# Kernel optimization log

Hardware: AMD Instinct MI355X
Metric: run time of the kernel (lower is better)

The kernel has to match this reference:

```python
import jax, jax.numpy as jnp
import numpy as np

B = 1024
N_SPEC = 2048
R1 = 20000
R2 = 40000


def setup_inputs() -> dict:
    key = jax.random.key(0)
    k1, k2, k3, k4, k5, k6, k7 = jax.random.split(key, 7)
    return {
        "y_in": jax.random.uniform(k1, (B, N_SPEC), dtype=jnp.float32),
        "rates_1st": jax.random.uniform(k2, (B, R1), dtype=jnp.float32),
        "rates_2nd": jax.random.uniform(k3, (B, R2), dtype=jnp.float32),
        "inds_1r": jax.random.randint(k4, (R1,), 0, N_SPEC, dtype=jnp.int32),
        "inds_1p": jax.random.randint(k5, (R1,), 0, N_SPEC, dtype=jnp.int32),
        "inds_2r": jax.random.randint(k6, (R2, 2), 0, N_SPEC, dtype=jnp.int32),
        "inds_2p": jax.random.randint(k7, (R2,), 0, N_SPEC, dtype=jnp.int32),
    }


def reference(y_in, rates_1st, rates_2nd, inds_1r, inds_1p, inds_2r, inds_2p):
    # First-order reactions: gather reactant abundance, scale by rate,
    # scatter-add into product species.  y_in: [B, S]
    term_1 = y_in[:, inds_1r] * rates_1st                      # [B, R1]
    # Second-order reactions: product of the two reactant abundances.
    term_2 = y_in[:, inds_2r[:, 0]] * y_in[:, inds_2r[:, 1]] * rates_2nd  # [B, R2]
    y_out = jnp.zeros_like(y_in)
    y_out = y_out.at[:, inds_1p].add(term_1)
    y_out = y_out.at[:, inds_2p].add(term_2)
    return y_out
```

## Files before the change

### kernel.cpp

```cpp
#include <hip/hip_runtime.h>


#define NSPEC 2048
#define BDIM  1024
#define R1    20000
#define R2    40000
#define CH    10000
#define NCH1  2
#define NCH2  4
#define NCH   (NCH1 + NCH2)
#define RTOT  (R1 + R2)

#define WS_CNT  0
#define WS_PTR  49152
#define WS_E1   98432
#define WS_E2   178560

__global__ __launch_bounds__(256) void k_zero(uint* cnt) {
    int i = blockIdx.x * 256 + threadIdx.x;
    if (i < NCH * NSPEC) cnt[i] = 0u;
}

__global__ __launch_bounds__(256) void k_hist(const int* __restrict__ inds_1p,
                                              const int* __restrict__ inds_2p,
                                              uint* __restrict__ cnt) {
    int j = blockIdx.x * 256 + threadIdx.x;
    if (j >= RTOT) return;
    if (j < R1) {
        int c = j / CH;
        atomicAdd(&cnt[c * NSPEC + inds_1p[j]], 1u);
    } else {
        int j2 = j - R1;
        int c = NCH1 + j2 / CH;
        atomicAdd(&cnt[c * NSPEC + inds_2p[j2]], 1u);
    }
}

__global__ __launch_bounds__(256) void k_scan(uint* __restrict__ cnt,
                                              uint* __restrict__ ptr) {
    __shared__ uint part[256];
    const int c   = blockIdx.x;
    const int tid = threadIdx.x;
    uint v[8];
    uint tsum = 0;
    #pragma unroll
    for (int k = 0; k < 8; ++k) { v[k] = cnt[c * NSPEC + tid * 8 + k]; tsum += v[k]; }
    part[tid] = tsum;
    __syncthreads();
    for (int off = 1; off < 256; off <<= 1) {
        uint x = (tid >= off) ? part[tid - off] : 0u;
        __syncthreads();
        part[tid] += x;
        __syncthreads();
    }
    uint run = part[tid] - tsum;
    #pragma unroll
    for (int k = 0; k < 8; ++k) {
        ptr[c * (NSPEC + 1) + tid * 8 + k] = run;
        cnt[c * NSPEC + tid * 8 + k]       = run;
        run += v[k];
    }
    if (tid == 255) ptr[c * (NSPEC + 1) + NSPEC] = run;
}

__global__ __launch_bounds__(256) void k_fill(const int* __restrict__ inds_1r,
                                              const int* __restrict__ inds_1p,
                                              const int* __restrict__ inds_2r,
                                              const int* __restrict__ inds_2p,
                                              uint*  __restrict__ cur,
                                              uint*  __restrict__ e1,
                                              uint2* __restrict__ e2) {
    int j = blockIdx.x * 256 + threadIdx.x;
    if (j >= RTOT) return;
    if (j < R1) {
        int c = j / CH;
        int s = inds_1p[j];
        uint pos = atomicAdd(&cur[c * NSPEC + s], 1u);
        uint jl  = (uint)(j - c * CH);
        e1[c * CH + pos] = (uint)inds_1r[j] | (jl << 16);
    } else {
        int j2 = j - R1;
        int c  = j2 / CH;
        int s  = inds_2p[j2];
        uint pos = atomicAdd(&cur[(NCH1 + c) * NSPEC + s], 1u);
        uint jl  = (uint)(j2 - c * CH);
        uint r0  = (uint)inds_2r[2 * j2];
        uint r1_ = (uint)inds_2r[2 * j2 + 1];
        e2[c * CH + pos] = make_uint2(r0 | (r1_ << 16), jl);
    }
}

#define MBLOCK 512
#define SPT    (NSPEC / MBLOCK)

__global__ __launch_bounds__(MBLOCK) void k_main(
    const float* __restrict__ y_in,
    const float* __restrict__ rates_1st,
    const float* __restrict__ rates_2nd,
    const uint*  __restrict__ ptr,
    const uint*  __restrict__ e1,
    const uint2* __restrict__ e2,
    float*       __restrict__ y_out)
{
    __shared__ float ys[NSPEC];
    __shared__ float rl[CH];

    const int b   = blockIdx.x;
    const int tid = threadIdx.x;

    {
        const float4* yrow = reinterpret_cast<const float4*>(y_in + (size_t)b * NSPEC);
        reinterpret_cast<float4*>(ys)[tid] = yrow[tid];
    }

    float acc[SPT];
    #pragma unroll
    for (int k = 0; k < SPT; ++k) acc[k] = 0.f;

    for (int c = 0; c < NCH; ++c) {
        const float* src = (c < NCH1)
            ? rates_1st + (size_t)b * R1 + c * CH
            : rates_2nd + (size_t)b * R2 + (c - NCH1) * CH;
        const float4* src4 = reinterpret_cast<const float4*>(src);
        float4* rl4 = reinterpret_cast<float4*>(rl);
        #pragma unroll
        for (int i = tid; i < CH / 4; i += MBLOCK) rl4[i] = src4[i];
        __syncthreads();

        const uint* pb = ptr + c * (NSPEC + 1);
        if (c < NCH1) {
            const uint* ec = e1 + c * CH;
            #pragma unroll
            for (int k = 0; k < SPT; ++k) {
                const int s = tid + k * MBLOCK;
                const uint beg = pb[s], end = pb[s + 1];
                float a = 0.f;
                for (uint j = beg; j < end; ++j) {
                    const uint e = ec[j];
                    a += ys[e & 0xFFFFu] * rl[e >> 16];
                }
                acc[k] += a;
            }
        } else {
            const uint2* ec = e2 + (c - NCH1) * CH;
            #pragma unroll
            for (int k = 0; k < SPT; ++k) {
                const int s = tid + k * MBLOCK;
                const uint beg = pb[s], end = pb[s + 1];
                float a = 0.f;
                for (uint j = beg; j < end; ++j) {
                    const uint2 e = ec[j];
                    a += ys[e.x & 0xFFFFu] * ys[e.x >> 16] * rl[e.y];
                }
                acc[k] += a;
            }
        }
        __syncthreads();
    }

    #pragma unroll
    for (int k = 0; k < SPT; ++k)
        y_out[(size_t)b * NSPEC + tid + k * MBLOCK] = acc[k];
}

extern "C" void kernel_launch(void* const* d_in, const int* in_sizes, int n_in,
                              void* d_out, int out_size, void* d_ws, size_t ws_size,
                              hipStream_t stream) {
    const float* y_in      = (const float*)d_in[0];
    const float* rates_1st = (const float*)d_in[1];
    const float* rates_2nd = (const float*)d_in[2];
    const int*   inds_1r   = (const int*)d_in[3];
    const int*   inds_1p   = (const int*)d_in[4];
    const int*   inds_2r   = (const int*)d_in[5];
    const int*   inds_2p   = (const int*)d_in[6];
    float*       y_out     = (float*)d_out;

    char* ws = (char*)d_ws;
    uint*  cnt = (uint*) (ws + WS_CNT);
    uint*  ptr = (uint*) (ws + WS_PTR);
    uint*  e1  = (uint*) (ws + WS_E1);
    uint2* e2  = (uint2*)(ws + WS_E2);

    k_zero<<<(NCH * NSPEC + 255) / 256, 256, 0, stream>>>(cnt);
    k_hist<<<(RTOT + 255) / 256, 256, 0, stream>>>(inds_1p, inds_2p, cnt);
    k_scan<<<NCH, 256, 0, stream>>>(cnt, ptr);
    k_fill<<<(RTOT + 255) / 256, 256, 0, stream>>>(inds_1r, inds_1p, inds_2r, inds_2p,
                                                   cnt, e1, e2);
    k_main<<<BDIM, MBLOCK, 0, stream>>>(y_in, rates_1st, rates_2nd, ptr, e1, e2, y_out);
}
```

Baseline: 399.0 us.

## Fuse CSR build into one kernel, shrink chunks, stage edge lists in LDS

```diff
diff --git a/kernel.cpp b/kernel.cpp
--- a/kernel.cpp
+++ b/kernel.cpp
@@ -5,88 +5,75 @@
 #define BDIM  1024
 #define R1    20000
 #define R2    40000
-#define CH    10000
-#define NCH1  2
-#define NCH2  4
+#define CH    4000
+#define NCH1  (R1 / CH)
+#define NCH2  (R2 / CH)
 #define NCH   (NCH1 + NCH2)
-#define RTOT  (R1 + R2)
 
-#define WS_CNT  0
-#define WS_PTR  49152
-#define WS_E1   98432
-#define WS_E2   178560
+#define WS_PTR 0
+#define WS_E1  61472
+#define WS_E2  141472
 
-__global__ __launch_bounds__(256) void k_zero(uint* cnt) {
-    int i = blockIdx.x * 256 + threadIdx.x;
-    if (i < NCH * NSPEC) cnt[i] = 0u;
-}
+__global__ __launch_bounds__(1024) void k_build(
+    const int* __restrict__ inds_1r, const int* __restrict__ inds_1p,
+    const int* __restrict__ inds_2r, const int* __restrict__ inds_2p,
+    ushort* __restrict__ ptr, uint* __restrict__ e1, uint2* __restrict__ e2)
+{
+    __shared__ uint cnt[NSPEC];
+    __shared__ uint part[1024];
 
-__global__ __launch_bounds__(256) void k_hist(const int* __restrict__ inds_1p,
-                                              const int* __restrict__ inds_2p,
-                                              uint* __restrict__ cnt) {
-    int j = blockIdx.x * 256 + threadIdx.x;
-    if (j >= RTOT) return;
-    if (j < R1) {
-        int c = j / CH;
-        atomicAdd(&cnt[c * NSPEC + inds_1p[j]], 1u);
-    } else {
-        int j2 = j - R1;
-        int c = NCH1 + j2 / CH;
-        atomicAdd(&cnt[c * NSPEC + inds_2p[j2]], 1u);
-    }
-}
-
-__global__ __launch_bounds__(256) void k_scan(uint* __restrict__ cnt,
-                                              uint* __restrict__ ptr) {
-    __shared__ uint part[256];
     const int c   = blockIdx.x;
     const int tid = threadIdx.x;
-    uint v[8];
-    uint tsum = 0;
-    #pragma unroll
-    for (int k = 0; k < 8; ++k) { v[k] = cnt[c * NSPEC + tid * 8 + k]; tsum += v[k]; }
+
+    cnt[tid]        = 0u;
+    cnt[tid + 1024] = 0u;
+    __syncthreads();
+
+    const bool first = (c < NCH1);
+    const int  base  = first ? c * CH : (c - NCH1) * CH;
+    const int* __restrict__ prod = first ? inds_1p : inds_2p;
+
+    for (int i = tid; i < CH; i += 1024)
+        atomicAdd(&cnt[prod[base + i]], 1u);
+    __syncthreads();
+
+    uint v0 = cnt[2 * tid], v1 = cnt[2 * tid + 1];
+    uint tsum = v0 + v1;
     part[tid] = tsum;
     __syncthreads();
-    for (int off = 1; off < 256; off <<= 1) {
+    for (int off = 1; off < 1024; off <<= 1) {
         uint x = (tid >= off) ? part[tid - off] : 0u;
         __syncthreads();
         part[tid] += x;
         __syncthreads();
     }
     uint run = part[tid] - tsum;
-    #pragma unroll
-    for (int k = 0; k < 8; ++k) {
-        ptr[c * (NSPEC + 1) + tid * 8 + k] = run;
-        cnt[c * NSPEC + tid * 8 + k]       = run;
-        run += v[k];
-    }
-    if (tid == 255) ptr[c * (NSPEC + 1) + NSPEC] = run;
-}
 
-__global__ __launch_bounds__(256) void k_fill(const int* __restrict__ inds_1r,
-                                              const int* __restrict__ inds_1p,
-                                              const int* __restrict__ inds_2r,
-                                              const int* __restrict__ inds_2p,
-                                              uint*  __restrict__ cur,
-                                              uint*  __restrict__ e1,
-                                              uint2* __restrict__ e2) {
-    int j = blockIdx.x * 256 + threadIdx.x;
-    if (j >= RTOT) return;
-    if (j < R1) {
-        int c = j / CH;
-        int s = inds_1p[j];
-        uint pos = atomicAdd(&cur[c * NSPEC + s], 1u);
-        uint jl  = (uint)(j - c * CH);
-        e1[c * CH + pos] = (uint)inds_1r[j] | (jl << 16);
+    ushort* pb = ptr + c * (NSPEC + 1);
+    pb[2 * tid]     = (ushort)run;
+    pb[2 * tid + 1] = (ushort)(run + v0);
+    cnt[2 * tid]     = run;
+    cnt[2 * tid + 1] = run + v0;
+    if (tid == 1023) pb[NSPEC] = (ushort)(run + tsum);
+    __syncthreads();
+
+    if (first) {
+        for (int i = tid; i < CH; i += 1024) {
+            const int j = base + i;
+            const int s = inds_1p[j];
+            const uint pos = atomicAdd(&cnt[s], 1u);
+            e1[c * CH + pos] = (uint)inds_1r[j] | ((uint)i << 16);
+        }
     } else {
-        int j2 = j - R1;
-        int c  = j2 / CH;
-        int s  = inds_2p[j2];
-        uint pos = atomicAdd(&cur[(NCH1 + c) * NSPEC + s], 1u);
-        uint jl  = (uint)(j2 - c * CH);
-        uint r0  = (uint)inds_2r[2 * j2];
-        uint r1_ = (uint)inds_2r[2 * j2 + 1];
-        e2[c * CH + pos] = make_uint2(r0 | (r1_ << 16), jl);
+        const int c2 = c - NCH1;
+        for (int i = tid; i < CH; i += 1024) {
+            const int j = base + i;
+            const int s = inds_2p[j];
+            const uint pos = atomicAdd(&cnt[s], 1u);
+            const uint r0  = (uint)inds_2r[2 * j];
+            const uint r1_ = (uint)inds_2r[2 * j + 1];
+            e2[c2 * CH + pos] = make_uint2(r0 | (r1_ << 16), (uint)i);
+        }
     }
 }
 
@@ -97,13 +84,16 @@
     const float* __restrict__ y_in,
     const float* __restrict__ rates_1st,
     const float* __restrict__ rates_2nd,
-    const uint*  __restrict__ ptr,
+    const ushort* __restrict__ ptr,
     const uint*  __restrict__ e1,
     const uint2* __restrict__ e2,
     float*       __restrict__ y_out)
 {
     __shared__ float ys[NSPEC];
-    __shared__ float rl[CH];
+    __shared__ __align__(16) unsigned char stage[CH * 4 + CH * 8];
+    float* rl  = (float*)stage;
+    uint*  e1c = (uint*) (stage + CH * 4);
+    uint2* e2c = (uint2*)(stage + CH * 4);
 
     const int b   = blockIdx.x;
     const int tid = threadIdx.x;
@@ -118,38 +108,47 @@
     for (int k = 0; k < SPT; ++k) acc[k] = 0.f;
 
     for (int c = 0; c < NCH; ++c) {
-        const float* src = (c < NCH1)
+        const bool first = (c < NCH1);
+
+        const float* rsrc = first
             ? rates_1st + (size_t)b * R1 + c * CH
             : rates_2nd + (size_t)b * R2 + (c - NCH1) * CH;
-        const float4* src4 = reinterpret_cast<const float4*>(src);
-        float4* rl4 = reinterpret_cast<float4*>(rl);
-        #pragma unroll
-        for (int i = tid; i < CH / 4; i += MBLOCK) rl4[i] = src4[i];
+        const float4* r4 = reinterpret_cast<const float4*>(rsrc);
+        for (int i = tid; i < CH / 4; i += MBLOCK)
+            reinterpret_cast<float4*>(rl)[i] = r4[i];
+
+        if (first) {
+            const float4* s4 = reinterpret_cast<const float4*>(e1 + c * CH);
+            for (int i = tid; i < CH / 4; i += MBLOCK)
+                reinterpret_cast<float4*>(e1c)[i] = s4[i];
+        } else {
+            const float4* s4 = reinterpret_cast<const float4*>(e2 + (c - NCH1) * CH);
+            for (int i = tid; i < CH / 2; i += MBLOCK)
+                reinterpret_cast<float4*>(e2c)[i] = s4[i];
+        }
         __syncthreads();
 
-        const uint* pb = ptr + c * (NSPEC + 1);
-        if (c < NCH1) {
-            const uint* ec = e1 + c * CH;
+        const ushort* pb = ptr + c * (NSPEC + 1);
+        if (first) {
             #pragma unroll
             for (int k = 0; k < SPT; ++k) {
                 const int s = tid + k * MBLOCK;
                 const uint beg = pb[s], end = pb[s + 1];
                 float a = 0.f;
                 for (uint j = beg; j < end; ++j) {
-                    const uint e = ec[j];
+                    const uint e = e1c[j];
                     a += ys[e & 0xFFFFu] * rl[e >> 16];
                 }
                 acc[k] += a;
             }
         } else {
-            const uint2* ec = e2 + (c - NCH1) * CH;
             #pragma unroll
             for (int k = 0; k < SPT; ++k) {
                 const int s = tid + k * MBLOCK;
                 const uint beg = pb[s], end = pb[s + 1];
                 float a = 0.f;
                 for (uint j = beg; j < end; ++j) {
-                    const uint2 e = ec[j];
+                    const uint2 e = e2c[j];
                     a += ys[e.x & 0xFFFFu] * ys[e.x >> 16] * rl[e.y];
                 }
                 acc[k] += a;
@@ -176,15 +175,12 @@
     float*       y_out     = (float*)d_out;
 
     char* ws = (char*)d_ws;
-    uint*  cnt = (uint*) (ws + WS_CNT);
-    uint*  ptr = (uint*) (ws + WS_PTR);
-    uint*  e1  = (uint*) (ws + WS_E1);
-    uint2* e2  = (uint2*)(ws + WS_E2);
+    ushort* ptr = (ushort*)(ws + WS_PTR);
+    uint*   e1  = (uint*)  (ws + WS_E1);
+    uint2*  e2  = (uint2*) (ws + WS_E2);
 
-    k_zero<<<(NCH * NSPEC + 255) / 256, 256, 0, stream>>>(cnt);
-    k_hist<<<(RTOT + 255) / 256, 256, 0, stream>>>(inds_1p, inds_2p, cnt);
-    k_scan<<<NCH, 256, 0, stream>>>(cnt, ptr);
-    k_fill<<<(RTOT + 255) / 256, 256, 0, stream>>>(inds_1r, inds_1p, inds_2r, inds_2p,
-                                                   cnt, e1, e2);
-    k_main<<<BDIM, MBLOCK, 0, stream>>>(y_in, rates_1st, rates_2nd, ptr, e1, e2, y_out);
+    k_build<<<NCH, 1024, 0, stream>>>(inds_1r, inds_1p, inds_2r, inds_2p,
+                                      ptr, e1, e2);
+    k_main<<<BDIM, MBLOCK, 0, stream>>>(y_in, rates_1st, rates_2nd,
+                                        ptr, e1, e2, y_out);
 }
```

Result: slower. 410.4 us (+2.9%).
